# Performance work log

Measured on AMD Instinct MI355X. Metric: run time of the kernel, lower is better.

Reference implementation:

```python
import jax, jax.numpy as jnp
import numpy as np

B, D, H, W, C = 2, 160, 192, 160, 1

def setup_inputs() -> dict:
    key = jax.random.key(0)
    k1, k2 = jax.random.split(key)
    vol = jax.random.normal(k1, (B, D, H, W, C), dtype=jnp.float32)
    # dense displacement field (voxel shifts), same spatial grid, 3 components
    loc_shift = jax.random.normal(k2, (B, D, H, W, 3), dtype=jnp.float32)
    return {"vol": vol, "loc_shift": loc_shift}

def _interp_trilinear(vol, loc):
    # vol: [D,H,W,C]; loc: [D,H,W,3] absolute sample coordinates (ij indexing).
    # fill_value=None in the original -> clamp coordinates to the volume domain
    # (nearest-neighbor extension), matching ne.utils.interpn's clipping.
    d, h, w, _ = vol.shape
    max_f = jnp.array([d - 1, h - 1, w - 1], dtype=loc.dtype)
    loc = jnp.clip(loc, 0.0, max_f)
    loc0 = jnp.floor(loc)
    diff = loc - loc0                      # trilinear weights in [0,1)
    i0 = loc0.astype(jnp.int32)
    i1 = jnp.minimum(i0 + 1, jnp.array([d - 1, h - 1, w - 1], jnp.int32))
    out = jnp.zeros_like(vol)
    for corner in range(8):                # fixed 8-corner loop (not a data-dim loop)
        bits = [(corner >> k) & 1 for k in range(3)]
        idx = [(i1 if bits[k] else i0)[..., k] for k in range(3)]
        wgt = jnp.ones(vol.shape[:3], dtype=vol.dtype)
        for k in range(3):
            wgt = wgt * (diff[..., k] if bits[k] else (1.0 - diff[..., k]))
        out = out + wgt[..., None] * vol[idx[0], idx[1], idx[2]]   # gather_nd
    return out

def reference(vol, loc_shift):
    # loc = identity grid + displacement (transform() semantics: sample at x + dx)
    d, h, w = vol.shape[1:4]
    grid = jnp.stack(
        jnp.meshgrid(jnp.arange(d, dtype=vol.dtype),
                     jnp.arange(h, dtype=vol.dtype),
                     jnp.arange(w, dtype=vol.dtype), indexing='ij'),
        axis=-1)                                    # [D,H,W,3]
    loc = grid[None] + loc_shift                    # [B,D,H,W,3]
    return jax.vmap(_interp_trilinear)(vol, loc)    # [B,D,H,W,C]
```

## Files before the change

### kernel.cpp

```cpp
#include <hip/hip_runtime.h>
#include <hip/hip_bf16.h>

#define BB 2
#define DD 160
#define HH 192
#define WW 160
#define SDp (HH * WW)

#define TD 11
#define TH 15
#define TWf 40
#define PLANE (TH * TWf)
#define TILE_F (TD * PLANE)
#define NF4 (TILE_F / 4)
#define NITER 7

__device__ __forceinline__ float2 ld2(const float* __restrict__ vb, int off) {
    float2 v;
    __builtin_memcpy(&v, vb + off, 8);
    return v;
}

__device__ __forceinline__ void gload_lds16(const float* g, float* l) {
    __builtin_amdgcn_global_load_lds(
        (const __attribute__((address_space(1))) void*)g,
        (__attribute__((address_space(3))) void*)l, 16, 0, 0);
}

__global__ void __launch_bounds__(256, 6)
st_trilinear_lds3(const float* __restrict__ vol,
                  const float* __restrict__ shift,
                  float* __restrict__ out) {
    __shared__ float tile[TILE_F];

    int bid = blockIdx.x;
    int xcd = bid & 7;
    int rank = bid >> 3;
    int zl = rank / 120;
    int xy = rank % 120;
    int by = xy / 5;
    int bx = xy - by * 5;
    int z = xcd * 10 + zl;
    int b = z / 40;
    int d0 = (z - b * 40) * 4;

    const int tid = threadIdx.y * 32 + threadIdx.x;
    const int w = bx * 32 + threadIdx.x;
    const int h = by * 8 + threadIdx.y;

    const int dlo = d0 - 3;
    const int hlo = by * 8 - 3;
    const int wlo = bx * 32 - 4;

    const float* __restrict__ vb = vol + (long)b * (DD * SDp);
    const long idx = (((long)b * DD + d0) * HH + h) * WW + w;

    float3 s0, s1, s2, s3;
    __builtin_memcpy(&s0, shift + (idx + 0 * SDp) * 3, 12);
    __builtin_memcpy(&s1, shift + (idx + 1 * SDp) * 3, 12);
    __builtin_memcpy(&s2, shift + (idx + 2 * SDp) * 3, 12);
    __builtin_memcpy(&s3, shift + (idx + 3 * SDp) * 3, 12);

    float* lbase = tile + (tid >> 6) * 256;
#pragma unroll
    for (int i = 0; i < NITER; ++i) {
        int e = i * 256 + tid;
        if (e < NF4) {
            int row = e / 10;
            int c4 = (e - row * 10) << 2;
            int dd = row / 15;
            int hh = row - dd * 15;
            int dsrc = min(max(dlo + dd, 0), DD - 1);
            int hsrc = min(max(hlo + hh, 0), HH - 1);
            int wsrc = min(max(wlo + c4, 0), WW - 4);
            gload_lds16(vb + dsrc * SDp + hsrc * WW + wsrc, lbase + i * 1024);
        }
    }
    __syncthreads();

    const float fd = (float)d0, fh = (float)h, fw = (float)w;

#pragma unroll
    for (int j = 0; j < 4; ++j) {
        float3 s = (j == 0) ? s0 : (j == 1) ? s1 : (j == 2) ? s2 : s3;

        float ldc = fminf(fmaxf(fd + (float)j + s.x, 0.0f), (float)(DD - 1));
        float lhc = fminf(fmaxf(fh + s.y, 0.0f), (float)(HH - 1));
        float lwc = fminf(fmaxf(fw + s.z, 0.0f), (float)(WW - 1));

        float fd0 = floorf(ldc), fh0 = floorf(lhc), fw0 = floorf(lwc);
        int d0c = (int)fd0, h0c = (int)fh0, w0c = (int)fw0;
        int d1c = min(d0c + 1, DD - 1);
        int h1c = min(h0c + 1, HH - 1);
        int wp  = min(w0c, WW - 2);

        float td_ = ldc - fd0;
        float th_ = lhc - fh0;
        float tw_ = (lwc - fw0) + (float)(w0c - wp);

        float2 a00, a01, a10, a11;
        bool ok = (d0c >= dlo) & (d1c <= dlo + TD - 1) &
                  (h0c >= hlo) & (h1c <= hlo + TH - 1) &
                  (wp >= wlo) & (wp + 1 <= wlo + TWf - 1);
        if (__builtin_expect(ok, 1)) {
            int lo  = ((d0c - dlo) * TH + (h0c - hlo)) * TWf + (wp - wlo);
            int d1l = (d1c - d0c) * PLANE;
            int h1l = (h1c - h0c) * TWf;
            a00 = make_float2(tile[lo], tile[lo + 1]);
            a01 = make_float2(tile[lo + h1l], tile[lo + h1l + 1]);
            a10 = make_float2(tile[lo + d1l], tile[lo + d1l + 1]);
            a11 = make_float2(tile[lo + d1l + h1l], tile[lo + d1l + h1l + 1]);
        } else {
            int go = d0c * SDp + h0c * WW + wp;
            int gd = (d1c - d0c) * SDp;
            int gh = (h1c - h0c) * WW;
            a00 = ld2(vb, go);
            a01 = ld2(vb, go + gh);
            a10 = ld2(vb, go + gd);
            a11 = ld2(vb, go + gd + gh);
        }

        float x00 = a00.x + tw_ * (a00.y - a00.x);
        float x01 = a01.x + tw_ * (a01.y - a01.x);
        float x10 = a10.x + tw_ * (a10.y - a10.x);
        float x11 = a11.x + tw_ * (a11.y - a11.x);
        float y0 = x00 + th_ * (x01 - x00);
        float y1 = x10 + th_ * (x11 - x10);
        float r = y0 + td_ * (y1 - y0);

        __builtin_nontemporal_store(r, out + idx + (long)j * SDp);
    }
}

extern "C" void kernel_launch(void* const* d_in, const int* in_sizes, int n_in,
                              void* d_out, int out_size, void* d_ws, size_t ws_size,
                              hipStream_t stream) {
    const float* vol   = (const float*)d_in[0];
    const float* shift = (const float*)d_in[1];
    float* out = (float*)d_out;

    dim3 block(32, 8, 1);
    int grid = (WW / 32) * (HH / 8) * (DD / 4) * BB;

    st_trilinear_lds3<<<grid, block, 0, stream>>>(vol, shift, out);
}
```

Before: 39.07 us.

## Store LDS tile as packed fp16 neighbor pairs loaded through registers

Replaces the direct global-to-LDS async copy with register loads. Each tile element is then stored as a packed fp16 pair of itself and its w+1 neighbour, so every trilinear corner pair needs one 32-bit LDS read instead of two. This halves LDS gather reads per sample. In exchange it adds conversion ALU work, an extra scalar global load per group, and register pressure. It also reduces precision to fp16 with round-toward-zero, which may fail tolerance checks.

New measurement: 43.16 us. 1.1x slower.

```diff
diff --git a/kernel.cpp b/kernel.cpp
--- a/kernel.cpp
+++ b/kernel.cpp
@@ -11,9 +11,21 @@
 #define TH 15
 #define TWf 40
 #define PLANE (TH * TWf)
-#define TILE_F (TD * PLANE)
-#define NF4 (TILE_F / 4)
+#define TILE_U (TD * PLANE)
+#define NGRP (TD * TH * (TWf/4))
 #define NITER 7
+
+typedef __fp16 half2v __attribute__((ext_vector_type(2)));
+
+__device__ __forceinline__ unsigned pk(float a, float b) {
+    half2v h = __builtin_amdgcn_cvt_pkrtz(a, b);
+    unsigned u; __builtin_memcpy(&u, &h, 4); return u;
+}
+
+__device__ __forceinline__ float2 unpk(unsigned u) {
+    half2v h; __builtin_memcpy(&h, &u, 4);
+    return make_float2((float)h[0], (float)h[1]);
+}
 
 __device__ __forceinline__ float2 ld2(const float* __restrict__ vb, int off) {
     float2 v;
@@ -21,17 +33,11 @@
     return v;
 }
 
-__device__ __forceinline__ void gload_lds16(const float* g, float* l) {
-    __builtin_amdgcn_global_load_lds(
-        (const __attribute__((address_space(1))) void*)g,
-        (__attribute__((address_space(3))) void*)l, 16, 0, 0);
-}
-
 __global__ void __launch_bounds__(256, 6)
-st_trilinear_lds3(const float* __restrict__ vol,
-                  const float* __restrict__ shift,
-                  float* __restrict__ out) {
-    __shared__ float tile[TILE_F];
+st_trilinear_pk(const float* __restrict__ vol,
+                const float* __restrict__ shift,
+                float* __restrict__ out) {
+    __shared__ __align__(16) unsigned tile[TILE_U];
 
     int bid = blockIdx.x;
     int xcd = bid & 7;
@@ -61,19 +67,34 @@
     __builtin_memcpy(&s2, shift + (idx + 2 * SDp) * 3, 12);
     __builtin_memcpy(&s3, shift + (idx + 3 * SDp) * 3, 12);
 
-    float* lbase = tile + (tid >> 6) * 256;
+    float4 A[NITER]; float bn[NITER]; int dst[NITER]; bool act[NITER];
 #pragma unroll
     for (int i = 0; i < NITER; ++i) {
         int e = i * 256 + tid;
-        if (e < NF4) {
-            int row = e / 10;
-            int c4 = (e - row * 10) << 2;
-            int dd = row / 15;
-            int hh = row - dd * 15;
-            int dsrc = min(max(dlo + dd, 0), DD - 1);
-            int hsrc = min(max(hlo + hh, 0), HH - 1);
-            int wsrc = min(max(wlo + c4, 0), WW - 4);
-            gload_lds16(vb + dsrc * SDp + hsrc * WW + wsrc, lbase + i * 1024);
+        act[i] = (e < NGRP);
+        int row = e / 10;
+        int c4 = (e - row * 10) << 2;
+        int dd = row / 15;
+        int hh = row - dd * 15;
+        int dsrc = min(max(dlo + dd, 0), DD - 1);
+        int hsrc = min(max(hlo + hh, 0), HH - 1);
+        int wsrc = min(max(wlo + c4, 0), WW - 4);
+        dst[i] = row * TWf + c4;
+        if (act[i]) {
+            const float* p = vb + dsrc * SDp + hsrc * WW + wsrc;
+            __builtin_memcpy(&A[i], p, 16);
+            bn[i] = *(vb + dsrc * SDp + hsrc * WW + min(wsrc + 4, WW - 1));
+        }
+    }
+#pragma unroll
+    for (int i = 0; i < NITER; ++i) {
+        if (act[i]) {
+            uint4 q;
+            q.x = pk(A[i].x, A[i].y);
+            q.y = pk(A[i].y, A[i].z);
+            q.z = pk(A[i].z, A[i].w);
+            q.w = pk(A[i].w, bn[i]);
+            *(uint4*)&tile[dst[i]] = q;
         }
     }
     __syncthreads();
@@ -106,10 +127,10 @@
             int lo  = ((d0c - dlo) * TH + (h0c - hlo)) * TWf + (wp - wlo);
             int d1l = (d1c - d0c) * PLANE;
             int h1l = (h1c - h0c) * TWf;
-            a00 = make_float2(tile[lo], tile[lo + 1]);
-            a01 = make_float2(tile[lo + h1l], tile[lo + h1l + 1]);
-            a10 = make_float2(tile[lo + d1l], tile[lo + d1l + 1]);
-            a11 = make_float2(tile[lo + d1l + h1l], tile[lo + d1l + h1l + 1]);
+            a00 = unpk(tile[lo]);
+            a01 = unpk(tile[lo + h1l]);
+            a10 = unpk(tile[lo + d1l]);
+            a11 = unpk(tile[lo + d1l + h1l]);
         } else {
             int go = d0c * SDp + h0c * WW + wp;
             int gd = (d1c - d0c) * SDp;
@@ -142,5 +163,5 @@
     dim3 block(32, 8, 1);
     int grid = (WW / 32) * (HH / 8) * (DD / 4) * BB;
 
-    st_trilinear_lds3<<<grid, block, 0, stream>>>(vol, shift, out);
+    st_trilinear_pk<<<grid, block, 0, stream>>>(vol, shift, out);
 }
```
